# Kernel tuning notes

Hardware: AMD Instinct MI355X
Metric: run time of the kernel (lower is better)

Reference implementation:

```python
import jax, jax.numpy as jnp
import numpy as np

B, H, P, D, NF = 16, 16, 128, 128, 12  # patches == head_dim required by lin_qk


def setup_inputs() -> dict:
    key = jax.random.key(0)
    ks = jax.random.split(key, 8)
    return {
        "q": jax.random.normal(ks[0], (B, H, P, D), jnp.float32),
        "k": jax.random.normal(ks[1], (B, H, P, D), jnp.float32),
        "scale": jnp.ones((1,), jnp.float32),  # unused by the original forward
        "grid": jnp.arange(NF, dtype=jnp.float32) + 1.0,
        "base_weight": jax.random.uniform(ks[2], (D, D), jnp.float32),
        "coef_q": jax.random.uniform(ks[3], (D, NF), jnp.float32),
        "coef_k": jax.random.uniform(ks[4], (D, NF), jnp.float32),
        "scale_base": jnp.ones((1, H, P, D), jnp.float32),
        "scale_sp": jnp.ones((1, H, P, D), jnp.float32),
        "w_qk": jax.random.normal(ks[5], (D, D), jnp.float32) / np.float32(np.sqrt(D)),
        "b_qk": jnp.zeros((D,), jnp.float32),
    }


def _branch(x, coef, grid, base_weight, scale_sp, scale_base):
    # base path: SiLU(x) @ W^T  (F.linear semantics)
    base = jax.nn.silu(x) @ base_weight.T
    # KAN sin basis: sin(grid_f * x_d) -> (B,H,P,NF,D); contract coef[d,f]
    s = jnp.sin(grid[:, None] * x[..., None, :])
    f = jnp.einsum('df,bhpfd->bhpd', coef, s)
    return jax.nn.sigmoid(f * scale_sp + base * scale_base)


def reference(q, k, scale, grid, base_weight, coef_q, coef_k, scale_base, scale_sp, w_qk, b_qk):
    # Per-channel sigmoids, then sum over D. The original builds the full
    # (B,H,P,P,D) broadcast tensor sig_q[...,p,None,:] + sig_k[...,None,p',:]
    # and sums over D; that is exactly separable:
    #   sum_d(sig_q[p,d]) + sum_d(sig_k[p',d])
    sq = _branch(q, coef_q, grid, base_weight, scale_sp, scale_base).sum(-1)  # (B,H,P)
    sk = _branch(k, coef_k, grid, base_weight, scale_sp, scale_base).sum(-1)  # (B,H,P)
    f_out = sq[..., :, None] + sk[..., None, :]  # (B,H,P,P)
    f_out = f_out @ w_qk.T + b_qk  # lin_qk: valid because patches == head_dim
    return jax.nn.softmax(f_out, axis=-1)
```

## Files before the change

kernel.cpp:

```cpp
#include <hip/hip_runtime.h>
#include <hip/hip_bf16.h>


typedef float          f32x4 __attribute__((ext_vector_type(4)));
typedef short          s16x8 __attribute__((ext_vector_type(8)));
typedef int            s32x4 __attribute__((ext_vector_type(4)));
typedef unsigned int   u32x4 __attribute__((ext_vector_type(4)));

#define LOG2E   1.44269504f
#define NLOG2E -1.44269504f
#define INV2PI  0.15915494309189535f

static __device__ __forceinline__ float hw_exp2(float x) {
    float r;
    asm("v_exp_f32 %0, %1" : "=v"(r) : "v"(x));
    return r;
}
static __device__ __forceinline__ float hw_sin_rev(float rev) {
    float f, r;
    asm("v_fract_f32 %0, %1" : "=v"(f) : "v"(rev));
    asm("v_sin_f32 %0, %1" : "=v"(r) : "v"(f));
    return r;
}
static __device__ __forceinline__ float fastrcp(float x) {
    return __builtin_amdgcn_rcpf(x);
}
static __device__ __forceinline__ unsigned int cvt_pk_bf16(float lo, float hi) {
    unsigned int r;
    asm("v_cvt_pk_bf16_f32 %0, %1, %2" : "=v"(r) : "v"(lo), "v"(hi));
    return r;
}
static __device__ __forceinline__ float sigmoid_fast(float z) {
    return fastrcp(1.f + hw_exp2(z * NLOG2E));
}
static __device__ __forceinline__ int swz(int local) {
    return local ^ (((local >> 8) & 7) << 4);
}

__global__ __launch_bounds__(512, 4) void k_branch(
    const float* __restrict__ q, const float* __restrict__ k,
    const float* __restrict__ bw,
    const float* __restrict__ gridv,
    const float* __restrict__ coef_q, const float* __restrict__ coef_k,
    const float* __restrict__ sbase,
    const float* __restrict__ ssp,
    float* __restrict__ sums_lo, float* __restrict__ sums_hi)
{
    __shared__ char smem[32768];
    float* F_l = (float*)smem;

    const int t = threadIdx.x;
    const int lane = t & 63, w = t >> 6;
    const int wr = w >> 1;
    const int ch = w & 1;
    const int r15 = lane & 15, g4 = lane >> 4;
    const int row0 = blockIdx.x * 64;
    const bool is_q = row0 < 32768;
    const float* X = is_q ? q : k;
    const float* coef = is_q ? coef_q : coef_k;
    const int xrow0 = is_q ? row0 : row0 - 32768;
    const float g1 = gridv[0];

    #pragma unroll
    for (int it = 0; it < 4; ++it) {
        int c = it * 512 + t;
        const float4* wp = (const float4*)&bw[(c >> 4) * 128 + (c & 15) * 8];
        float4 w0 = wp[0], w1 = wp[1];
        u32x4 v = {cvt_pk_bf16(w0.x, w0.y), cvt_pk_bf16(w0.z, w0.w),
                   cvt_pk_bf16(w1.x, w1.y), cvt_pk_bf16(w1.z, w1.w)};
        *(u32x4*)(smem + swz(c * 16)) = v;
    }
    __syncthreads();

    const float* xrowp = &X[(xrow0 + wr * 16 + r15) * 128];

    f32x4 acc[4];
    #pragma unroll
    for (int n = 0; n < 4; ++n) acc[n] = (f32x4){0.f, 0.f, 0.f, 0.f};

    #pragma unroll
    for (int s = 0; s < 4; ++s) {
        const float4* xp = (const float4*)&xrowp[s * 32 + g4 * 8];
        float4 x0 = xp[0], x1 = xp[1];
        float xsv[8] = {x0.x, x0.y, x0.z, x0.w, x1.x, x1.y, x1.z, x1.w};
        float sl[8];
        #pragma unroll
        for (int j = 0; j < 8; ++j) {
            float e = hw_exp2(xsv[j] * NLOG2E);
            sl[j] = xsv[j] * fastrcp(1.f + e);
        }
        s32x4 a4 = {(int)cvt_pk_bf16(sl[0], sl[1]), (int)cvt_pk_bf16(sl[2], sl[3]),
                    (int)cvt_pk_bf16(sl[4], sl[5]), (int)cvt_pk_bf16(sl[6], sl[7])};
        s16x8 af = __builtin_bit_cast(s16x8, a4);
        #pragma unroll
        for (int n = 0; n < 4; ++n) {
            s16x8 bf = *(const s16x8*)(smem + swz((ch * 64 + n * 16 + r15) * 256
                                                  + s * 64 + g4 * 16));
            acc[n] = __builtin_amdgcn_mfma_f32_16x16x32_bf16(af, bf, acc[n], 0, 0, 0);
        }
    }
    __syncthreads();

    #pragma unroll
    for (int n = 0; n < 4; ++n) {
        int cl = n * 16 + r15;
        #pragma unroll
        for (int reg = 0; reg < 4; ++reg) {
            int rl = g4 * 4 + reg;
            F_l[(wr * 16 + rl) * 128 + ch * 64 + ((cl + rl * 4) & 63)] = acc[n][reg];
        }
    }

    const int ce = lane & 15;
    const int re = lane >> 4;
    float cf[4][12];
    #pragma unroll
    for (int j = 0; j < 4; ++j) {
        const float4* cp = (const float4*)&coef[(ch * 64 + ce * 4 + j) * 12];
        float4 c0 = cp[0], c1 = cp[1], c2 = cp[2];
        cf[j][0] = c0.x; cf[j][1] = c0.y; cf[j][2]  = c0.z; cf[j][3]  = c0.w;
        cf[j][4] = c1.x; cf[j][5] = c1.y; cf[j][6]  = c1.z; cf[j][7]  = c1.w;
        cf[j][8] = c2.x; cf[j][9] = c2.y; cf[j][10] = c2.z; cf[j][11] = c2.w;
    }

    const float grev = g1 * INV2PI;
    #pragma unroll
    for (int i = 0; i < 4; ++i) {
        int rl = re * 4 + i;
        int rb = wr * 16 + rl;
        int grow = row0 + rb;
        int hp = grow & 2047;
        int gcol = ch * 64 + ce * 4;
        f32x4 F4 = *(f32x4*)&F_l[rb * 128 + ch * 64 + ((ce * 4 + rl * 4) & 63)];
        float4 x4 = *(const float4*)&X[(xrow0 + rb) * 128 + gcol];
        float4 sp = *(const float4*)&ssp[hp * 128 + gcol];
        float4 sb = *(const float4*)&sbase[hp * 128 + gcol];
        float xv[4]  = {x4.x, x4.y, x4.z, x4.w};
        float spv[4] = {sp.x, sp.y, sp.z, sp.w};
        float sbv[4] = {sb.x, sb.y, sb.z, sb.w};
        float ps = 0.f;
        #pragma unroll
        for (int j = 0; j < 4; ++j) {
            float rev = grev * xv[j];
            float s1 = hw_sin_rev(rev);
            float cv = hw_sin_rev(rev + 0.25f);
            float t2 = cv + cv;
            float sprev = 0.f, scur = s1;
            float f = cf[j][0] * s1;
            #pragma unroll
            for (int u = 1; u < 12; ++u) {
                float sn = __builtin_fmaf(t2, scur, -sprev);
                f = __builtin_fmaf(cf[j][u], sn, f);
                sprev = scur; scur = sn;
            }
            float z = f * spv[j] + F4[j] * sbv[j];
            ps += sigmoid_fast(z);
        }
        ps += __shfl_xor(ps, 1, 64);
        ps += __shfl_xor(ps, 2, 64);
        ps += __shfl_xor(ps, 4, 64);
        ps += __shfl_xor(ps, 8, 64);
        if (ce == 0) (ch ? sums_hi : sums_lo)[grow] = ps;
    }
}

__global__ __launch_bounds__(256) void k_attn(
    const float* __restrict__ sums_lo, const float* __restrict__ sums_hi,
    const float* __restrict__ w_qk, const float* __restrict__ b_qk,
    float* __restrict__ out)
{
    __shared__ float skl[128], Tl[128], Rl[128];
    const int bh = blockIdx.x >> 1;
    const int half = blockIdx.x & 1;
    const int t = threadIdx.x;

    if (t < 128) {
        int idx = 32768 + bh * 128 + t;
        skl[t] = sums_lo[idx] + sums_hi[idx];
    }
    __syncthreads();
    if (t < 128) {
        const float4* wr = (const float4*)&w_qk[t * 128];
        float a = 0.f, r = 0.f;
        #pragma unroll 8
        for (int p4 = 0; p4 < 32; ++p4) {
            float4 w4 = wr[p4];
            a += w4.x * skl[p4 * 4 + 0] + w4.y * skl[p4 * 4 + 1] +
                 w4.z * skl[p4 * 4 + 2] + w4.w * skl[p4 * 4 + 3];
            r += w4.x + w4.y + w4.z + w4.w;
        }
        Tl[t] = a + b_qk[t];
        Rl[t] = r;
    }
    __syncthreads();

    const int lane = t & 63, w = t >> 6;
    #pragma unroll
    for (int it = 0; it < 16; ++it) {
        int row = bh * 128 + half * 64 + it * 4 + w;
        float sqv = sums_lo[row] + sums_hi[row];
        float2 r2 = *(const float2*)&Rl[lane * 2];
        float2 t2 = *(const float2*)&Tl[lane * 2];
        float l0 = __builtin_fmaf(sqv, r2.x, t2.x);
        float l1 = __builtin_fmaf(sqv, r2.y, t2.y);
        float m = fmaxf(l0, l1);
        #pragma unroll
        for (int s = 32; s >= 1; s >>= 1) m = fmaxf(m, __shfl_xor(m, s, 64));
        float e0 = hw_exp2((l0 - m) * LOG2E);
        float e1 = hw_exp2((l1 - m) * LOG2E);
        float sum = e0 + e1;
        #pragma unroll
        for (int w2 = 32; w2 >= 1; w2 >>= 1) sum += __shfl_xor(sum, w2, 64);
        float inv = fastrcp(sum);
        float2 o2 = {e0 * inv, e1 * inv};
        *(float2*)&out[row * 128 + lane * 2] = o2;
    }
}

extern "C" void kernel_launch(void* const* d_in, const int* in_sizes, int n_in,
                              void* d_out, int out_size, void* d_ws, size_t ws_size,
                              hipStream_t stream) {
    (void)in_sizes; (void)n_in; (void)out_size; (void)ws_size;
    const float* q      = (const float*)d_in[0];
    const float* k      = (const float*)d_in[1];
    const float* gridv  = (const float*)d_in[3];
    const float* bw     = (const float*)d_in[4];
    const float* coef_q = (const float*)d_in[5];
    const float* coef_k = (const float*)d_in[6];
    const float* sbase  = (const float*)d_in[7];
    const float* ssp    = (const float*)d_in[8];
    const float* w_qk   = (const float*)d_in[9];
    const float* b_qk   = (const float*)d_in[10];

    float* out  = (float*)d_out;
    float* ws      = (float*)d_ws;
    float* sums_lo = ws;
    float* sums_hi = ws + 65536;

    k_branch<<<1024, 512, 0, stream>>>(q, k, bw, gridv, coef_q, coef_k,
                                       sbase, ssp, sums_lo, sums_hi);
    k_attn<<<512, 256, 0, stream>>>(sums_lo, sums_hi, w_qk, b_qk, out);
}
```

Before: 42.80 us.

## Pre-convert base weight to bf16, reorder KAN loop, split attn matvec

```diff
diff --git a/kernel.cpp b/kernel.cpp
--- a/kernel.cpp
+++ b/kernel.cpp
@@ -6,6 +6,7 @@
 typedef short          s16x8 __attribute__((ext_vector_type(8)));
 typedef int            s32x4 __attribute__((ext_vector_type(4)));
 typedef unsigned int   u32x4 __attribute__((ext_vector_type(4)));
+typedef unsigned short u16x8 __attribute__((ext_vector_type(8)));
 
 #define LOG2E   1.44269504f
 #define NLOG2E -1.44269504f
@@ -37,9 +38,20 @@
     return local ^ (((local >> 8) & 7) << 4);
 }
 
+__global__ __launch_bounds__(256) void k_convert(const float* __restrict__ bw,
+                                                 unsigned short* __restrict__ wbf) {
+    int i = blockIdx.x * 256 + threadIdx.x;
+    if (i < 128 * 128) {
+        __hip_bfloat16 h = __float2bfloat16(bw[i]);
+        unsigned short r;
+        __builtin_memcpy(&r, &h, 2);
+        wbf[i] = r;
+    }
+}
+
 __global__ __launch_bounds__(512, 4) void k_branch(
     const float* __restrict__ q, const float* __restrict__ k,
-    const float* __restrict__ bw,
+    const unsigned short* __restrict__ wbf,
     const float* __restrict__ gridv,
     const float* __restrict__ coef_q, const float* __restrict__ coef_k,
     const float* __restrict__ sbase,
@@ -64,11 +76,8 @@
     #pragma unroll
     for (int it = 0; it < 4; ++it) {
         int c = it * 512 + t;
-        const float4* wp = (const float4*)&bw[(c >> 4) * 128 + (c & 15) * 8];
-        float4 w0 = wp[0], w1 = wp[1];
-        u32x4 v = {cvt_pk_bf16(w0.x, w0.y), cvt_pk_bf16(w0.z, w0.w),
-                   cvt_pk_bf16(w1.x, w1.y), cvt_pk_bf16(w1.z, w1.w)};
-        *(u32x4*)(smem + swz(c * 16)) = v;
+        u16x8 v = *(const u16x8*)&wbf[c * 8];
+        *(u16x8*)(smem + swz(c * 16)) = v;
     }
     __syncthreads();
 
@@ -113,54 +122,62 @@
 
     const int ce = lane & 15;
     const int re = lane >> 4;
-    float cf[4][12];
-    #pragma unroll
-    for (int j = 0; j < 4; ++j) {
-        const float4* cp = (const float4*)&coef[(ch * 64 + ce * 4 + j) * 12];
-        float4 c0 = cp[0], c1 = cp[1], c2 = cp[2];
-        cf[j][0] = c0.x; cf[j][1] = c0.y; cf[j][2]  = c0.z; cf[j][3]  = c0.w;
-        cf[j][4] = c1.x; cf[j][5] = c1.y; cf[j][6]  = c1.z; cf[j][7]  = c1.w;
-        cf[j][8] = c2.x; cf[j][9] = c2.y; cf[j][10] = c2.z; cf[j][11] = c2.w;
-    }
-
-    const float grev = g1 * INV2PI;
+    const int gcol = ch * 64 + ce * 4;
+
+    float Fr[16], xr[16], spr[16], sbr[16];
     #pragma unroll
     for (int i = 0; i < 4; ++i) {
         int rl = re * 4 + i;
         int rb = wr * 16 + rl;
-        int grow = row0 + rb;
-        int hp = grow & 2047;
-        int gcol = ch * 64 + ce * 4;
+        int hp = (row0 + rb) & 2047;
         f32x4 F4 = *(f32x4*)&F_l[rb * 128 + ch * 64 + ((ce * 4 + rl * 4) & 63)];
         float4 x4 = *(const float4*)&X[(xrow0 + rb) * 128 + gcol];
         float4 sp = *(const float4*)&ssp[hp * 128 + gcol];
         float4 sb = *(const float4*)&sbase[hp * 128 + gcol];
-        float xv[4]  = {x4.x, x4.y, x4.z, x4.w};
-        float spv[4] = {sp.x, sp.y, sp.z, sp.w};
-        float sbv[4] = {sb.x, sb.y, sb.z, sb.w};
-        float ps = 0.f;
-        #pragma unroll
-        for (int j = 0; j < 4; ++j) {
-            float rev = grev * xv[j];
+        Fr[i*4+0]=F4[0]; Fr[i*4+1]=F4[1]; Fr[i*4+2]=F4[2]; Fr[i*4+3]=F4[3];
+        xr[i*4+0]=x4.x;  xr[i*4+1]=x4.y;  xr[i*4+2]=x4.z;  xr[i*4+3]=x4.w;
+        spr[i*4+0]=sp.x; spr[i*4+1]=sp.y; spr[i*4+2]=sp.z; spr[i*4+3]=sp.w;
+        sbr[i*4+0]=sb.x; sbr[i*4+1]=sb.y; sbr[i*4+2]=sb.z; sbr[i*4+3]=sb.w;
+    }
+
+    const float grev = g1 * INV2PI;
+    float ps[4] = {0.f, 0.f, 0.f, 0.f};
+    #pragma unroll
+    for (int j = 0; j < 4; ++j) {
+        const float4* cp = (const float4*)&coef[(gcol + j) * 12];
+        float4 c0 = cp[0], c1 = cp[1], c2 = cp[2];
+        float cf[12] = {c0.x, c0.y, c0.z, c0.w, c1.x, c1.y, c1.z, c1.w,
+                        c2.x, c2.y, c2.z, c2.w};
+        #pragma unroll
+        for (int i = 0; i < 4; ++i) {
+            float xv = xr[i*4+j];
+            float rev = grev * xv;
             float s1 = hw_sin_rev(rev);
             float cv = hw_sin_rev(rev + 0.25f);
             float t2 = cv + cv;
             float sprev = 0.f, scur = s1;
-            float f = cf[j][0] * s1;
+            float f = cf[0] * s1;
             #pragma unroll
             for (int u = 1; u < 12; ++u) {
                 float sn = __builtin_fmaf(t2, scur, -sprev);
-                f = __builtin_fmaf(cf[j][u], sn, f);
+                f = __builtin_fmaf(cf[u], sn, f);
                 sprev = scur; scur = sn;
             }
-            float z = f * spv[j] + F4[j] * sbv[j];
-            ps += sigmoid_fast(z);
-        }
-        ps += __shfl_xor(ps, 1, 64);
-        ps += __shfl_xor(ps, 2, 64);
-        ps += __shfl_xor(ps, 4, 64);
-        ps += __shfl_xor(ps, 8, 64);
-        if (ce == 0) (ch ? sums_hi : sums_lo)[grow] = ps;
+            float z = f * spr[i*4+j] + Fr[i*4+j] * sbr[i*4+j];
+            ps[i] += sigmoid_fast(z);
+        }
+    }
+    #pragma unroll
+    for (int i = 0; i < 4; ++i) {
+        float v = ps[i];
+        v += __shfl_xor(v, 1, 64);
+        v += __shfl_xor(v, 2, 64);
+        v += __shfl_xor(v, 4, 64);
+        v += __shfl_xor(v, 8, 64);
+        if (ce == 0) {
+            int grow = row0 + wr * 16 + re * 4 + i;
+            (ch ? sums_hi : sums_lo)[grow] = v;
+        }
     }
 }
 
@@ -169,7 +186,7 @@
     const float* __restrict__ w_qk, const float* __restrict__ b_qk,
     float* __restrict__ out)
 {
-    __shared__ float skl[128], Tl[128], Rl[128];
+    __shared__ float skl[128], Tp[2][128], Rp[2][128], Tl[128], Rl[128];
     const int bh = blockIdx.x >> 1;
     const int half = blockIdx.x & 1;
     const int t = threadIdx.x;
@@ -179,18 +196,25 @@
         skl[t] = sums_lo[idx] + sums_hi[idx];
     }
     __syncthreads();
-    if (t < 128) {
-        const float4* wr = (const float4*)&w_qk[t * 128];
+    {
+        int j = t & 127, ph = t >> 7;
+        const float4* wr = (const float4*)&w_qk[j * 128 + ph * 64];
+        const float* sk2 = &skl[ph * 64];
         float a = 0.f, r = 0.f;
         #pragma unroll 8
-        for (int p4 = 0; p4 < 32; ++p4) {
+        for (int p4 = 0; p4 < 16; ++p4) {
             float4 w4 = wr[p4];
-            a += w4.x * skl[p4 * 4 + 0] + w4.y * skl[p4 * 4 + 1] +
-                 w4.z * skl[p4 * 4 + 2] + w4.w * skl[p4 * 4 + 3];
+            a += w4.x * sk2[p4 * 4 + 0] + w4.y * sk2[p4 * 4 + 1] +
+                 w4.z * sk2[p4 * 4 + 2] + w4.w * sk2[p4 * 4 + 3];
             r += w4.x + w4.y + w4.z + w4.w;
         }
-        Tl[t] = a + b_qk[t];
-        Rl[t] = r;
+        Tp[ph][j] = a;
+        Rp[ph][j] = r;
+    }
+    __syncthreads();
+    if (t < 128) {
+        Tl[t] = Tp[0][t] + Tp[1][t] + b_qk[t];
+        Rl[t] = Rp[0][t] + Rp[1][t];
     }
     __syncthreads();
 
@@ -236,8 +260,10 @@
     float* ws      = (float*)d_ws;
     float* sums_lo = ws;
     float* sums_hi = ws + 65536;
-
-    k_branch<<<1024, 512, 0, stream>>>(q, k, bw, gridv, coef_q, coef_k,
+    unsigned short* wbf = (unsigned short*)(ws + 131072);
+
+    k_convert<<<64, 256, 0, stream>>>(bw, wbf);
+    k_branch<<<1024, 512, 0, stream>>>(q, k, wbf, gridv, coef_q, coef_k,
                                        sbase, ssp, sums_lo, sums_hi);
     k_attn<<<512, 256, 0, stream>>>(sums_lo, sums_hi, w_qk, b_qk, out);
 }
```

Measured after the change: 42.83 us. About the same (+0.1%).
